# Optimization experiments

Measured on AMD Instinct MI355X. Metric: run time of the kernel, lower is better.

Reference implementation:

```python
import jax, jax.numpy as jnp
import numpy as np
from math import sqrt, log

N_PATCHES = 128
ATTN_WINDOW = 10
NEG_INF = -10000.0


def _causal_mask(L):
    # patch id per position; query patch i may attend key patch j iff 0 < (j_pid - i_pid) < window
    channels = L // N_PATCHES
    pid = jnp.repeat(jnp.arange(N_PATCHES), channels)  # [L]
    diff = pid[None, :] - pid[:, None]                 # [L_query, L_key] = pid[key]-pid[query]
    return (diff <= 0) | (diff >= ATTN_WINDOW)         # True => blocked


def setup_inputs() -> dict:
    key = jax.random.key(0)
    kq, kk, kv = jax.random.split(key, 3)
    B, H, L, D = 4, 8, 1024, 64
    return {
        "queries": jax.random.normal(kq, (B, H, L, D), dtype=jnp.float32),
        "keys": jax.random.normal(kk, (B, H, L, D), dtype=jnp.float32),
        "values": jax.random.normal(kv, (B, H, L, D), dtype=jnp.float32),
        "log_scale": jnp.asarray(np.log(2.0), dtype=jnp.float32),
    }


def reference(queries, keys, values, log_scale):
    B, H, L, D = queries.shape
    scores = jnp.einsum("bhld,bhmd->bhlm", queries, keys)           # [B,H,L,L]
    scale = jnp.clip(jnp.exp(log_scale), 1.0, 30.0) / sqrt(D)
    mask = _causal_mask(L)                                          # [L,L]
    pos = jnp.where(mask, NEG_INF, scores)
    neg = jnp.where(mask, NEG_INF, -scores)
    A = jax.nn.softmax(scale * pos, axis=-1) - jax.nn.softmax(scale * neg, axis=-1)
    V = jnp.einsum("bhlm,bhmd->bhld", A, values)
    return V
```

## Files before the change

kernel.cpp:

```cpp
#include <hip/hip_runtime.h>
#include <math.h>

#define NPATCH 128
#define CH 8
#define D 64
#define G 8
#define NQ (G*CH)
#define NKEY 128
#define QSTR 72
#define KSTR 72
#define VSTR 136
#define PSTR 136

typedef __fp16 half8 __attribute__((ext_vector_type(8)));
typedef float  f32x4 __attribute__((ext_vector_type(4)));
typedef unsigned u32x4 __attribute__((ext_vector_type(4)));

static __device__ __forceinline__ unsigned pk(float x, float y) {
    return __builtin_bit_cast(unsigned, __builtin_amdgcn_cvt_pkrtz(x, y));
}
static __device__ __forceinline__ half8 ld8(const unsigned short* p) {
    return __builtin_bit_cast(half8, *(const u32x4*)p);
}

__global__ __launch_bounds__(256) void signed_attn_kernel(
    const float* __restrict__ Q, const float* __restrict__ K,
    const float* __restrict__ V, const float* __restrict__ logscale,
    float* __restrict__ O)
{
    __shared__ __align__(16) unsigned short sQ[NQ * QSTR];
    __shared__ __align__(16) unsigned short sK[NKEY * KSTR];
    __shared__ __align__(16) unsigned short sVt[D * VSTR];
    __shared__ __align__(16) unsigned short sP[NQ * PSTR];

    const int tid = threadIdx.x;
    const int grp = blockIdx.x & 15;
    const int bh  = blockIdx.x >> 4;
    const int p0  = grp * G;

    const long long base = (long long)bh * (NPATCH * CH) * D;
    const int nst = min(NKEY, (NPATCH - 1 - p0) * CH);

    const float scale = fminf(fmaxf(__expf(logscale[0]), 1.0f), 30.0f) * 0.125f;

    const float4* Qg = (const float4*)(Q + base + (long long)(p0 * CH) * D);
    for (int i = tid; i < NQ * 16; i += 256) {
        const int row = i >> 4, d4 = i & 15;
        const float4 v = Qg[i];
        *(uint2*)&sQ[row * QSTR + d4 * 4] = make_uint2(pk(v.x, v.y), pk(v.z, v.w));
    }
    const float4* Kg = (const float4*)(K + base + (long long)((p0 + 1) * CH) * D);
    for (int i = tid; i < NKEY * 16; i += 256) {
        const int row = i >> 4, d4 = i & 15;
        uint2 w = make_uint2(0u, 0u);
        if (row < nst) { const float4 v = Kg[i]; w = make_uint2(pk(v.x, v.y), pk(v.z, v.w)); }
        *(uint2*)&sK[row * KSTR + d4 * 4] = w;
    }
    const float4* Vg = (const float4*)(V + base + (long long)((p0 + 1) * CH) * D);
    for (int u = tid; u < 64 * 16; u += 256) {
        const int kp = u & 63, dq = u >> 6;
        float4 va = make_float4(0.f, 0.f, 0.f, 0.f);
        float4 vb = va;
        if (2 * kp < nst) { va = Vg[(2 * kp) * 16 + dq]; vb = Vg[(2 * kp + 1) * 16 + dq]; }
        *(unsigned*)&sVt[(dq * 4 + 0) * VSTR + 2 * kp] = pk(va.x, vb.x);
        *(unsigned*)&sVt[(dq * 4 + 1) * VSTR + 2 * kp] = pk(va.y, vb.y);
        *(unsigned*)&sVt[(dq * 4 + 2) * VSTR + 2 * kp] = pk(va.z, vb.z);
        *(unsigned*)&sVt[(dq * 4 + 3) * VSTR + 2 * kp] = pk(va.w, vb.w);
    }
    __syncthreads();

    const int wav = tid >> 6, lane = tid & 63;
    const int col = lane & 15, quad = lane >> 4;

    const half8 a0 = ld8(&sQ[(wav * 16 + col) * QSTR + quad * 8]);
    const half8 a1 = ld8(&sQ[(wav * 16 + col) * QSTR + 32 + quad * 8]);

    f32x4 acc[8];
#pragma unroll
    for (int t = 0; t < 8; ++t) acc[t] = (f32x4){0.f, 0.f, 0.f, 0.f};
#pragma unroll
    for (int t = 0; t < 8; ++t) {
        const half8 b0 = ld8(&sK[(t * 16 + col) * KSTR + quad * 8]);
        const half8 b1 = ld8(&sK[(t * 16 + col) * KSTR + 32 + quad * 8]);
        acc[t] = __builtin_amdgcn_mfma_f32_16x16x32_f16(a0, b0, acc[t], 0, 0, 0);
        acc[t] = __builtin_amdgcn_mfma_f32_16x16x32_f16(a1, b1, acc[t], 0, 0, 0);
    }

#pragma unroll
    for (int r = 0; r < 4; ++r) {
        const int q   = wav * 16 + quad * 4 + r;
        const int kr0 = (q >> 3) * 8;
        const int kmx = min(kr0 + 72, nst);

        float tv[8]; bool vl[8];
        float mp = -1e30f, mn = -1e30f;
#pragma unroll
        for (int t = 0; t < 8; ++t) {
            const int c = col + 16 * t;
            tv[t] = scale * acc[t][r];
            vl[t] = (c >= kr0) && (c < kmx);
            mp = fmaxf(mp, vl[t] ?  tv[t] : -1e30f);
            mn = fmaxf(mn, vl[t] ? -tv[t] : -1e30f);
        }
#pragma unroll
        for (int off = 1; off < 16; off <<= 1) {
            mp = fmaxf(mp, __shfl_xor(mp, off));
            mn = fmaxf(mn, __shfl_xor(mn, off));
        }
        float ep[8], en[8], sp = 0.f, sn = 0.f;
#pragma unroll
        for (int t = 0; t < 8; ++t) {
            ep[t] = vl[t] ? __expf( tv[t] - mp) : 0.f;
            en[t] = vl[t] ? __expf(-tv[t] - mn) : 0.f;
            sp += ep[t]; sn += en[t];
        }
#pragma unroll
        for (int off = 1; off < 16; off <<= 1) {
            sp += __shfl_xor(sp, off);
            sn += __shfl_xor(sn, off);
        }
        const float rp = (sp > 0.f) ? 1.f / sp : 0.f;
        const float rn = (sn > 0.f) ? 1.f / sn : 0.f;
#pragma unroll
        for (int t = 0; t < 8; ++t) {
            const float A = ep[t] * rp - en[t] * rn;
            sP[q * PSTR + col + 16 * t] = (unsigned short)pk(A, A);
        }
    }

    f32x4 oc[4];
#pragma unroll
    for (int t = 0; t < 4; ++t) oc[t] = (f32x4){0.f, 0.f, 0.f, 0.f};
#pragma unroll
    for (int kq = 0; kq < 4; ++kq) {
        const half8 ap = ld8(&sP[(wav * 16 + col) * PSTR + kq * 32 + quad * 8]);
#pragma unroll
        for (int t = 0; t < 4; ++t) {
            const half8 bv = ld8(&sVt[(t * 16 + col) * VSTR + kq * 32 + quad * 8]);
            oc[t] = __builtin_amdgcn_mfma_f32_16x16x32_f16(ap, bv, oc[t], 0, 0, 0);
        }
    }

    float* Ob = O + base + (long long)(p0 * CH) * D;
#pragma unroll
    for (int t = 0; t < 4; ++t) {
#pragma unroll
        for (int r = 0; r < 4; ++r) {
            Ob[(wav * 16 + quad * 4 + r) * D + t * 16 + col] = oc[t][r];
        }
    }
}

extern "C" void kernel_launch(void* const* d_in, const int* in_sizes, int n_in,
                              void* d_out, int out_size, void* d_ws, size_t ws_size,
                              hipStream_t stream) {
    const float* Q  = (const float*)d_in[0];
    const float* K  = (const float*)d_in[1];
    const float* V  = (const float*)d_in[2];
    const float* ls = (const float*)d_in[3];
    float* O = (float*)d_out;

    const int L = 1024;
    const int nBH = in_sizes[0] / (L * D);
    dim3 grid(nBH * (NPATCH / G));
    signed_attn_kernel<<<grid, 256, 0, stream>>>(Q, K, V, ls, O);
}
```

Measured before the change: 83.48 us.

## Skip fully masked key tiles per wave and load Q directly into registers

Each wave now computes scores only for the 5 key tiles of 16 that can fall inside its band window, not all 8. It also runs the PV product over 3 k-chunks instead of 4, with P stored in a narrower band-relative layout and V offsets clamped. Q is read straight from global memory into MFMA registers, which removes the Q shared-memory tile and overlaps that load with the K/V staging before the barrier. The aim is to cut wasted MFMA, exp and LDS work on masked regions. The cost is extra indexing complexity and a clamped V offset whose correctness depends on the zero-padded P columns.

After: 82.50 us. Within noise of the previous version (-1.2%).

```diff
diff --git a/kernel.cpp b/kernel.cpp
--- a/kernel.cpp
+++ b/kernel.cpp
@@ -7,10 +7,9 @@
 #define G 8
 #define NQ (G*CH)
 #define NKEY 128
-#define QSTR 72
 #define KSTR 72
 #define VSTR 136
-#define PSTR 136
+#define PSTR 100
 
 typedef __fp16 half8 __attribute__((ext_vector_type(8)));
 typedef float  f32x4 __attribute__((ext_vector_type(4)));
@@ -22,13 +21,16 @@
 static __device__ __forceinline__ half8 ld8(const unsigned short* p) {
     return __builtin_bit_cast(half8, *(const u32x4*)p);
 }
+static __device__ __forceinline__ half8 mk8(const float4& a, const float4& b) {
+    u32x4 u = { pk(a.x, a.y), pk(a.z, a.w), pk(b.x, b.y), pk(b.z, b.w) };
+    return __builtin_bit_cast(half8, u);
+}
 
 __global__ __launch_bounds__(256) void signed_attn_kernel(
     const float* __restrict__ Q, const float* __restrict__ K,
     const float* __restrict__ V, const float* __restrict__ logscale,
     float* __restrict__ O)
 {
-    __shared__ __align__(16) unsigned short sQ[NQ * QSTR];
     __shared__ __align__(16) unsigned short sK[NKEY * KSTR];
     __shared__ __align__(16) unsigned short sVt[D * VSTR];
     __shared__ __align__(16) unsigned short sP[NQ * PSTR];
@@ -43,45 +45,44 @@
 
     const float scale = fminf(fmaxf(__expf(logscale[0]), 1.0f), 30.0f) * 0.125f;
 
-    const float4* Qg = (const float4*)(Q + base + (long long)(p0 * CH) * D);
-    for (int i = tid; i < NQ * 16; i += 256) {
-        const int row = i >> 4, d4 = i & 15;
-        const float4 v = Qg[i];
-        *(uint2*)&sQ[row * QSTR + d4 * 4] = make_uint2(pk(v.x, v.y), pk(v.z, v.w));
+    {
+        const float4* Kg = (const float4*)(K + base + (long long)((p0 + 1) * CH) * D);
+        for (int i = tid; i < NKEY * 16; i += 256) {
+            const int row = i >> 4, d4 = i & 15;
+            uint2 w = make_uint2(0u, 0u);
+            if (row < nst) { const float4 v = Kg[i]; w = make_uint2(pk(v.x, v.y), pk(v.z, v.w)); }
+            *(uint2*)&sK[row * KSTR + d4 * 4] = w;
+        }
+        const float4* Vg = (const float4*)(V + base + (long long)((p0 + 1) * CH) * D);
+        for (int u = tid; u < 64 * 16; u += 256) {
+            const int kp = u & 63, dq = u >> 6;
+            float4 va = make_float4(0.f, 0.f, 0.f, 0.f);
+            float4 vb = va;
+            if (2 * kp < nst) { va = Vg[(2 * kp) * 16 + dq]; vb = Vg[(2 * kp + 1) * 16 + dq]; }
+            *(unsigned*)&sVt[(dq * 4 + 0) * VSTR + 2 * kp] = pk(va.x, vb.x);
+            *(unsigned*)&sVt[(dq * 4 + 1) * VSTR + 2 * kp] = pk(va.y, vb.y);
+            *(unsigned*)&sVt[(dq * 4 + 2) * VSTR + 2 * kp] = pk(va.z, vb.z);
+            *(unsigned*)&sVt[(dq * 4 + 3) * VSTR + 2 * kp] = pk(va.w, vb.w);
+        }
     }
-    const float4* Kg = (const float4*)(K + base + (long long)((p0 + 1) * CH) * D);
-    for (int i = tid; i < NKEY * 16; i += 256) {
-        const int row = i >> 4, d4 = i & 15;
-        uint2 w = make_uint2(0u, 0u);
-        if (row < nst) { const float4 v = Kg[i]; w = make_uint2(pk(v.x, v.y), pk(v.z, v.w)); }
-        *(uint2*)&sK[row * KSTR + d4 * 4] = w;
-    }
-    const float4* Vg = (const float4*)(V + base + (long long)((p0 + 1) * CH) * D);
-    for (int u = tid; u < 64 * 16; u += 256) {
-        const int kp = u & 63, dq = u >> 6;
-        float4 va = make_float4(0.f, 0.f, 0.f, 0.f);
-        float4 vb = va;
-        if (2 * kp < nst) { va = Vg[(2 * kp) * 16 + dq]; vb = Vg[(2 * kp + 1) * 16 + dq]; }
-        *(unsigned*)&sVt[(dq * 4 + 0) * VSTR + 2 * kp] = pk(va.x, vb.x);
-        *(unsigned*)&sVt[(dq * 4 + 1) * VSTR + 2 * kp] = pk(va.y, vb.y);
-        *(unsigned*)&sVt[(dq * 4 + 2) * VSTR + 2 * kp] = pk(va.z, vb.z);
-        *(unsigned*)&sVt[(dq * 4 + 3) * VSTR + 2 * kp] = pk(va.w, vb.w);
-    }
-    __syncthreads();
 
     const int wav = tid >> 6, lane = tid & 63;
     const int col = lane & 15, quad = lane >> 4;
 
-    const half8 a0 = ld8(&sQ[(wav * 16 + col) * QSTR + quad * 8]);
-    const half8 a1 = ld8(&sQ[(wav * 16 + col) * QSTR + 32 + quad * 8]);
+    const float4* Qg4 = (const float4*)(Q + base + (long long)(p0 * CH + wav * 16 + col) * D);
+    const half8 a0 = mk8(Qg4[quad * 2],     Qg4[quad * 2 + 1]);
+    const half8 a1 = mk8(Qg4[8 + quad * 2], Qg4[9 + quad * 2]);
 
-    f32x4 acc[8];
+    __syncthreads();
+
+    f32x4 acc[5];
 #pragma unroll
-    for (int t = 0; t < 8; ++t) acc[t] = (f32x4){0.f, 0.f, 0.f, 0.f};
+    for (int t = 0; t < 5; ++t) acc[t] = (f32x4){0.f, 0.f, 0.f, 0.f};
 #pragma unroll
-    for (int t = 0; t < 8; ++t) {
-        const half8 b0 = ld8(&sK[(t * 16 + col) * KSTR + quad * 8]);
-        const half8 b1 = ld8(&sK[(t * 16 + col) * KSTR + 32 + quad * 8]);
+    for (int t = 0; t < 5; ++t) {
+        const int krow = (wav + t) * 16 + col;
+        const half8 b0 = ld8(&sK[krow * KSTR + quad * 8]);
+        const half8 b1 = ld8(&sK[krow * KSTR + 32 + quad * 8]);
         acc[t] = __builtin_amdgcn_mfma_f32_16x16x32_f16(a0, b0, acc[t], 0, 0, 0);
         acc[t] = __builtin_amdgcn_mfma_f32_16x16x32_f16(a1, b1, acc[t], 0, 0, 0);
     }
@@ -92,11 +93,11 @@
         const int kr0 = (q >> 3) * 8;
         const int kmx = min(kr0 + 72, nst);
 
-        float tv[8]; bool vl[8];
+        float tv[5]; bool vl[5];
         float mp = -1e30f, mn = -1e30f;
 #pragma unroll
-        for (int t = 0; t < 8; ++t) {
-            const int c = col + 16 * t;
+        for (int t = 0; t < 5; ++t) {
+            const int c = (wav + t) * 16 + col;
             tv[t] = scale * acc[t][r];
             vl[t] = (c >= kr0) && (c < kmx);
             mp = fmaxf(mp, vl[t] ?  tv[t] : -1e30f);
@@ -107,9 +108,9 @@
             mp = fmaxf(mp, __shfl_xor(mp, off));
             mn = fmaxf(mn, __shfl_xor(mn, off));
         }
-        float ep[8], en[8], sp = 0.f, sn = 0.f;
+        float ep[5], en[5], sp = 0.f, sn = 0.f;
 #pragma unroll
-        for (int t = 0; t < 8; ++t) {
+        for (int t = 0; t < 5; ++t) {
             ep[t] = vl[t] ? __expf( tv[t] - mp) : 0.f;
             en[t] = vl[t] ? __expf(-tv[t] - mn) : 0.f;
             sp += ep[t]; sn += en[t];
@@ -122,21 +123,24 @@
         const float rp = (sp > 0.f) ? 1.f / sp : 0.f;
         const float rn = (sn > 0.f) ? 1.f / sn : 0.f;
 #pragma unroll
-        for (int t = 0; t < 8; ++t) {
+        for (int t = 0; t < 5; ++t) {
             const float A = ep[t] * rp - en[t] * rn;
-            sP[q * PSTR + col + 16 * t] = (unsigned short)pk(A, A);
+            sP[q * PSTR + t * 16 + col] = (unsigned short)pk(A, A);
         }
+        sP[q * PSTR + 80 + col] = 0;
     }
 
     f32x4 oc[4];
 #pragma unroll
     for (int t = 0; t < 4; ++t) oc[t] = (f32x4){0.f, 0.f, 0.f, 0.f};
 #pragma unroll
-    for (int kq = 0; kq < 4; ++kq) {
+    for (int kq = 0; kq < 3; ++kq) {
         const half8 ap = ld8(&sP[(wav * 16 + col) * PSTR + kq * 32 + quad * 8]);
+        const int kb = wav * 16 + kq * 32 + quad * 8;
+        const int kcl = (kb <= 120) ? kb : 120;
 #pragma unroll
         for (int t = 0; t < 4; ++t) {
-            const half8 bv = ld8(&sVt[(t * 16 + col) * VSTR + kq * 32 + quad * 8]);
+            const half8 bv = ld8(&sVt[(t * 16 + col) * VSTR + kcl]);
             oc[t] = __builtin_amdgcn_mfma_f32_16x16x32_f16(ap, bv, oc[t], 0, 0, 0);
         }
     }
```
